# Kernel tuning notes

Hardware: AMD Instinct MI355X
Metric: run time of the kernel (lower is better)

The kernel has to match this reference:

```python
import jax, jax.numpy as jnp
import numpy as np

T, B, I, H = 512, 64, 128, 1024


def setup_inputs() -> dict:
    key = jax.random.key(0)
    k1, k2, k3, k4 = jax.random.split(key, 4)
    # scale recurrent weights to keep tanh in a reasonable regime (spectral-radius-ish)
    return {
        "x": jax.random.normal(k1, (T, B, I), dtype=jnp.float32),
        "h0": jnp.zeros((B, H), dtype=jnp.float32),
        "w_ih": jax.random.normal(k2, (H, I), dtype=jnp.float32) / np.sqrt(I),
        "w_hh": jax.random.normal(k3, (H, H), dtype=jnp.float32) * (0.9 / np.sqrt(H)),
        "b": jax.random.normal(k4, (H,), dtype=jnp.float32) * 0.1,
    }


def reference(x, h0, w_ih, w_hh, b):
    # ESNLayer: python loop over time -> lax.scan with the recurrent carry.
    # cell: h_t = tanh(x_t @ W_ih^T + h_{t-1} @ W_hh^T + b); out_t = h_t
    def step(h, x_t):
        h_new = jnp.tanh(x_t @ w_ih.T + h @ w_hh.T + b)  # [B, H]
        return h_new, h_new

    h_final, outputs = jax.lax.scan(step, h0, x)  # outputs: [T, B, H]
    return outputs, h_final
```

## Files before the change

kernel.cpp:

```cpp
#include <hip/hip_runtime.h>
#include <math.h>


#define T_STEPS 512
#define BATCH   64
#define HDIM    1024
#define IDIM    128
#define KDIM    1152
#define NWG     256
#define NB      8

typedef float f32x4_t __attribute__((ext_vector_type(4)));

__device__ __forceinline__ unsigned sc_load(const unsigned* p) {
    unsigned v;
    asm volatile("global_load_dword %0, %1, off sc0 sc1\n\ts_waitcnt vmcnt(0)"
                 : "=&v"(v) : "v"(p) : "memory");
    return v;
}

__device__ __forceinline__ void sc_load4x4(const float* p0, const float* p1,
                                           const float* p2, const float* p3,
                                           float4& a, float4& b,
                                           float4& c, float4& d) {
    asm volatile(
        "global_load_dwordx4 %0, %4, off sc0 sc1\n\t"
        "global_load_dwordx4 %1, %5, off sc0 sc1\n\t"
        "global_load_dwordx4 %2, %6, off sc0 sc1\n\t"
        "global_load_dwordx4 %3, %7, off sc0 sc1\n\t"
        "s_waitcnt vmcnt(0)"
        : "=&v"(a), "=&v"(b), "=&v"(c), "=&v"(d)
        : "v"(p0), "v"(p1), "v"(p2), "v"(p3)
        : "memory");
}

__device__ __forceinline__ void sc_store4(float* p, float4 v) {
    f32x4_t t;
    t.x = v.x; t.y = v.y; t.z = v.z; t.w = v.w;
    asm volatile("global_store_dwordx4 %0, %1, off sc0 sc1\n\ts_waitcnt vmcnt(0)"
                 :: "v"(p), "v"(t) : "memory");
}

__device__ __forceinline__ void flag_store(unsigned* p, unsigned v) {
    asm volatile("global_store_dword %0, %1, off sc0 sc1"
                 :: "v"(p), "v"(v) : "memory");
}

__global__ void transpose_f32(const float* __restrict__ src, float* __restrict__ dst,
                              int R, int C) {
    __shared__ float tile[64][65];
    const int tcol = threadIdx.x & 63;
    const int trow = threadIdx.x >> 6;
    const int nbx = C >> 6;
    const int bx = blockIdx.x % nbx;
    const int by = blockIdx.x / nbx;
    const int c0 = bx << 6, r0 = by << 6;
    for (int i = trow; i < 64; i += 4)
        tile[i][tcol] = src[(size_t)(r0 + i) * C + c0 + tcol];
    __syncthreads();
    for (int i = trow; i < 64; i += 4)
        dst[(size_t)(c0 + i) * R + r0 + tcol] = tile[tcol][i];
}

__global__ __launch_bounds__(512) void esn_persistent(
    const float* __restrict__ x,
    const float* __restrict__ h0,
    const float* __restrict__ WT,
    const float* __restrict__ bias,
    float* __restrict__ out,
    float* __restrict__ hfin,
    unsigned* flags)
{
    const int tid  = threadIdx.x;
    const int wg   = blockIdx.x;
    const int wave = tid >> 6;
    const int lane = tid & 63;
    const int jq   = lane & 7;
    const int ksub = lane >> 3;
    const int jblk = ((wg & 7) << 2) | ((wg >> 3) & 3);
    const int bgrp = wg >> 5;
    const int b0   = bgrp << 3;
    const int j0   = (jblk << 5) + (jq << 2);
    const int krec = wave << 7;
    const int kx   = HDIM + (wave << 4) + (ksub << 1);

    __shared__ float  ht2[8 * 1024];
    __shared__ float  htx[8 * 128];
    __shared__ float4 red[2][8 * 8 * 9];

    float4 Wv[18];
    {
        const float* wp = WT + (size_t)krec * HDIM + j0;
        #pragma unroll
        for (int i = 0; i < 4; ++i) {
            const int kk = ((i << 3) + ksub) << 2;
            const float* wk = wp + (size_t)kk * HDIM;
            Wv[i * 4 + 0] = *(const float4*)(wk);
            Wv[i * 4 + 1] = *(const float4*)(wk + HDIM);
            Wv[i * 4 + 2] = *(const float4*)(wk + 2 * HDIM);
            Wv[i * 4 + 3] = *(const float4*)(wk + 3 * HDIM);
        }
        const float* wkx = WT + (size_t)kx * HDIM + j0;
        Wv[16] = *(const float4*)(wkx);
        Wv[17] = *(const float4*)(wkx + HDIM);
    }

    float4 b4 = make_float4(0.f, 0.f, 0.f, 0.f);
    int jj = 0;
    if (lane < 8) {
        jj = (jblk << 5) + (lane << 2);
        b4 = *(const float4*)(bias + jj);
    }

    unsigned* fl_pub = flags + (bgrp << 8) + (jblk << 3) + wave;
    const unsigned* fl_poll = flags + (bgrp << 8) + (wave << 5) + (lane & 31);

    const int sbb = lane >> 5;
    const int sko = (lane & 31) << 2;
    float* hdst = ht2 + (wave << 10) + (lane << 2);
    const int xr = lane >> 3;
    const int xco = (lane & 7) << 1;
    float* xdst = htx + (wave << 7) + (xr << 4) + xco;
    const float* hb = ht2 + (wave << 10);
    const float* xb = htx + (wave << 7);

    float2 xv2 = *(const float2*)(x + (size_t)(b0 + xr) * IDIM + (wave << 4) + xco);

    for (int t = 0; t < T_STEPS; ++t) {
        *(float2*)xdst = xv2;
        if (t == 0) {
            const float* p = h0 + (size_t)(b0 + sbb) * HDIM + krec + sko;
            *(float4*)(hdst)       = *(const float4*)(p);
            *(float4*)(hdst + 256) = *(const float4*)(p + 2 * HDIM);
            *(float4*)(hdst + 512) = *(const float4*)(p + 4 * HDIM);
            *(float4*)(hdst + 768) = *(const float4*)(p + 6 * HDIM);
        } else {
            unsigned f;
            do { f = sc_load(fl_poll); } while (!__all((int)(f >= (unsigned)t)));
            const float* p = out + ((size_t)(t - 1) * BATCH + b0 + sbb) * HDIM
                             + krec + sko;
            float4 a, b, c, d;
            sc_load4x4(p, p + 2 * HDIM, p + 4 * HDIM, p + 6 * HDIM, a, b, c, d);
            *(float4*)(hdst)       = a;
            *(float4*)(hdst + 256) = b;
            *(float4*)(hdst + 512) = c;
            *(float4*)(hdst + 768) = d;
        }

        if (t + 1 < T_STEPS)
            xv2 = *(const float2*)(x + ((size_t)(t + 1) * BATCH + b0 + xr) * IDIM
                                   + (wave << 4) + xco);

        float4 acc[NB];
        #pragma unroll
        for (int bb = 0; bb < NB; ++bb) acc[bb] = make_float4(0.f, 0.f, 0.f, 0.f);

        #pragma unroll
        for (int i = 0; i < 4; ++i) {
            const int ko = ((i << 3) + ksub) << 2;
            const float4 w0 = Wv[i * 4 + 0], w1 = Wv[i * 4 + 1];
            const float4 w2 = Wv[i * 4 + 2], w3 = Wv[i * 4 + 3];
            #pragma unroll
            for (int bb = 0; bb < NB; ++bb) {
                float4 h4 = *(const float4*)(hb + (bb << 7) + ko);
                acc[bb].x = fmaf(w0.x, h4.x, acc[bb].x);
                acc[bb].y = fmaf(w0.y, h4.x, acc[bb].y);
                acc[bb].z = fmaf(w0.z, h4.x, acc[bb].z);
                acc[bb].w = fmaf(w0.w, h4.x, acc[bb].w);
                acc[bb].x = fmaf(w1.x, h4.y, acc[bb].x);
                acc[bb].y = fmaf(w1.y, h4.y, acc[bb].y);
                acc[bb].z = fmaf(w1.z, h4.y, acc[bb].z);
                acc[bb].w = fmaf(w1.w, h4.y, acc[bb].w);
                acc[bb].x = fmaf(w2.x, h4.z, acc[bb].x);
                acc[bb].y = fmaf(w2.y, h4.z, acc[bb].y);
                acc[bb].z = fmaf(w2.z, h4.z, acc[bb].z);
                acc[bb].w = fmaf(w2.w, h4.z, acc[bb].w);
                acc[bb].x = fmaf(w3.x, h4.w, acc[bb].x);
                acc[bb].y = fmaf(w3.y, h4.w, acc[bb].y);
                acc[bb].z = fmaf(w3.z, h4.w, acc[bb].z);
                acc[bb].w = fmaf(w3.w, h4.w, acc[bb].w);
            }
        }
        #pragma unroll
        for (int bb = 0; bb < NB; ++bb) {
            float2 hx = *(const float2*)(xb + (bb << 4) + (ksub << 1));
            acc[bb].x = fmaf(Wv[16].x, hx.x, acc[bb].x);
            acc[bb].y = fmaf(Wv[16].y, hx.x, acc[bb].y);
            acc[bb].z = fmaf(Wv[16].z, hx.x, acc[bb].z);
            acc[bb].w = fmaf(Wv[16].w, hx.x, acc[bb].w);
            acc[bb].x = fmaf(Wv[17].x, hx.y, acc[bb].x);
            acc[bb].y = fmaf(Wv[17].y, hx.y, acc[bb].y);
            acc[bb].z = fmaf(Wv[17].z, hx.y, acc[bb].z);
            acc[bb].w = fmaf(Wv[17].w, hx.y, acc[bb].w);
        }

        #pragma unroll
        for (int bb = 0; bb < NB; ++bb) {
            acc[bb].x += __shfl_xor(acc[bb].x, 8);
            acc[bb].y += __shfl_xor(acc[bb].y, 8);
            acc[bb].z += __shfl_xor(acc[bb].z, 8);
            acc[bb].w += __shfl_xor(acc[bb].w, 8);
            acc[bb].x += __shfl_xor(acc[bb].x, 16);
            acc[bb].y += __shfl_xor(acc[bb].y, 16);
            acc[bb].z += __shfl_xor(acc[bb].z, 16);
            acc[bb].w += __shfl_xor(acc[bb].w, 16);
            acc[bb].x += __shfl_xor(acc[bb].x, 32);
            acc[bb].y += __shfl_xor(acc[bb].y, 32);
            acc[bb].z += __shfl_xor(acc[bb].z, 32);
            acc[bb].w += __shfl_xor(acc[bb].w, 32);
        }
        if (ksub == 0) {
            #pragma unroll
            for (int bb = 0; bb < NB; ++bb)
                red[t & 1][((wave << 3) + jq) * 9 + bb] = acc[bb];
        }
        __syncthreads();

        if (lane < 8) {
            float4 s = make_float4(0.f, 0.f, 0.f, 0.f);
            #pragma unroll
            for (int w = 0; w < 8; ++w) {
                float4 r = red[t & 1][((w << 3) + lane) * 9 + wave];
                s.x += r.x; s.y += r.y; s.z += r.z; s.w += r.w;
            }
            float4 o;
            o.x = tanhf(s.x + b4.x);
            o.y = tanhf(s.y + b4.y);
            o.z = tanhf(s.z + b4.z);
            o.w = tanhf(s.w + b4.w);
            sc_store4(out + ((size_t)t * BATCH + b0 + wave) * HDIM + jj, o);
            if (t == T_STEPS - 1)
                *(float4*)(hfin + (size_t)(b0 + wave) * HDIM + jj) = o;
        }
        if (lane == 0)
            flag_store(fl_pub, (unsigned)(t + 1));
    }
}

extern "C" void kernel_launch(void* const* d_in, const int* in_sizes, int n_in,
                              void* d_out, int out_size, void* d_ws, size_t ws_size,
                              hipStream_t stream) {
    const float* x    = (const float*)d_in[0];
    const float* h0   = (const float*)d_in[1];
    const float* w_ih = (const float*)d_in[2];
    const float* w_hh = (const float*)d_in[3];
    const float* bias = (const float*)d_in[4];
    float* out = (float*)d_out;

    char* ws = (char*)d_ws;
    float*    WT    = (float*)ws;
    unsigned* flags = (unsigned*)(ws + 4718592);

    (void)hipMemsetAsync(flags, 0, 8192, stream);
    transpose_f32<<<256, 256, 0, stream>>>(w_hh, WT, HDIM, HDIM);
    transpose_f32<<<32, 256, 0, stream>>>(w_ih, WT + (size_t)HDIM * HDIM, HDIM, IDIM);
    esn_persistent<<<NWG, 512, 0, stream>>>(x, h0, WT, bias,
                                            out, out + (size_t)T_STEPS * BATCH * HDIM,
                                            flags);
}
```

Before: 3.115 ms.

## Use L2-scoped coherence when a batch group's workgroups share one XCD

Workgroups are remapped so each batch group is wg&7, which under round-robin dispatch likely places all 32 workgroups of a group on the same XCD. At startup each group records its XCC IDs through atomics. If they all share one XCD, the flag polls, hidden-state loads and output stores use sc0-only (L2-coherent) accesses instead of sc0 sc1 system-scope bypass, which cuts per-step synchronisation latency. Flag stores are issued twice, and every 16th poll still uses full bypass as a safety net. This adds a startup barrier, extra workspace, and relies on the assumption about hardware dispatch order.

After: 8.399 ms. 2.7x slower.

```diff
diff --git a/kernel.cpp b/kernel.cpp
--- a/kernel.cpp
+++ b/kernel.cpp
@@ -12,38 +12,62 @@
 
 typedef float f32x4_t __attribute__((ext_vector_type(4)));
 
-__device__ __forceinline__ unsigned sc_load(const unsigned* p) {
+__device__ __forceinline__ unsigned flag_load(const unsigned* p, bool slow) {
     unsigned v;
-    asm volatile("global_load_dword %0, %1, off sc0 sc1\n\ts_waitcnt vmcnt(0)"
-                 : "=&v"(v) : "v"(p) : "memory");
+    if (slow)
+        asm volatile("global_load_dword %0, %1, off sc0 sc1\n\ts_waitcnt vmcnt(0)"
+                     : "=&v"(v) : "v"(p) : "memory");
+    else
+        asm volatile("global_load_dword %0, %1, off sc0\n\ts_waitcnt vmcnt(0)"
+                     : "=&v"(v) : "v"(p) : "memory");
     return v;
 }
 
-__device__ __forceinline__ void sc_load4x4(const float* p0, const float* p1,
-                                           const float* p2, const float* p3,
-                                           float4& a, float4& b,
-                                           float4& c, float4& d) {
-    asm volatile(
-        "global_load_dwordx4 %0, %4, off sc0 sc1\n\t"
-        "global_load_dwordx4 %1, %5, off sc0 sc1\n\t"
-        "global_load_dwordx4 %2, %6, off sc0 sc1\n\t"
-        "global_load_dwordx4 %3, %7, off sc0 sc1\n\t"
-        "s_waitcnt vmcnt(0)"
-        : "=&v"(a), "=&v"(b), "=&v"(c), "=&v"(d)
-        : "v"(p0), "v"(p1), "v"(p2), "v"(p3)
-        : "memory");
-}
-
-__device__ __forceinline__ void sc_store4(float* p, float4 v) {
+__device__ __forceinline__ void h_load4x4(const float* p0, const float* p1,
+                                          const float* p2, const float* p3,
+                                          float4& a, float4& b,
+                                          float4& c, float4& d, bool byp) {
+    if (byp)
+        asm volatile(
+            "global_load_dwordx4 %0, %4, off sc0 sc1\n\t"
+            "global_load_dwordx4 %1, %5, off sc0 sc1\n\t"
+            "global_load_dwordx4 %2, %6, off sc0 sc1\n\t"
+            "global_load_dwordx4 %3, %7, off sc0 sc1\n\t"
+            "s_waitcnt vmcnt(0)"
+            : "=&v"(a), "=&v"(b), "=&v"(c), "=&v"(d)
+            : "v"(p0), "v"(p1), "v"(p2), "v"(p3)
+            : "memory");
+    else
+        asm volatile(
+            "global_load_dwordx4 %0, %4, off sc0\n\t"
+            "global_load_dwordx4 %1, %5, off sc0\n\t"
+            "global_load_dwordx4 %2, %6, off sc0\n\t"
+            "global_load_dwordx4 %3, %7, off sc0\n\t"
+            "s_waitcnt vmcnt(0)"
+            : "=&v"(a), "=&v"(b), "=&v"(c), "=&v"(d)
+            : "v"(p0), "v"(p1), "v"(p2), "v"(p3)
+            : "memory");
+}
+
+__device__ __forceinline__ void out_store4(float* p, float4 v, bool byp) {
     f32x4_t t;
     t.x = v.x; t.y = v.y; t.z = v.z; t.w = v.w;
-    asm volatile("global_store_dwordx4 %0, %1, off sc0 sc1\n\ts_waitcnt vmcnt(0)"
-                 :: "v"(p), "v"(t) : "memory");
-}
-
-__device__ __forceinline__ void flag_store(unsigned* p, unsigned v) {
-    asm volatile("global_store_dword %0, %1, off sc0 sc1"
-                 :: "v"(p), "v"(v) : "memory");
+    if (byp)
+        asm volatile("global_store_dwordx4 %0, %1, off sc0 sc1\n\ts_waitcnt vmcnt(0)"
+                     :: "v"(p), "v"(t) : "memory");
+    else
+        asm volatile("global_store_dwordx4 %0, %1, off sc0\n\ts_waitcnt vmcnt(0)"
+                     :: "v"(p), "v"(t) : "memory");
+}
+
+__device__ __forceinline__ void flag_store(unsigned* p, unsigned v, bool byp) {
+    if (byp)
+        asm volatile("global_store_dword %0, %1, off sc0 sc1"
+                     :: "v"(p), "v"(v) : "memory");
+    else
+        asm volatile("global_store_dword %0, %1, off sc0\n\t"
+                     "global_store_dword %0, %1, off sc0 sc1"
+                     :: "v"(p), "v"(v) : "memory");
 }
 
 __global__ void transpose_f32(const float* __restrict__ src, float* __restrict__ dst,
@@ -77,8 +101,8 @@
     const int lane = tid & 63;
     const int jq   = lane & 7;
     const int ksub = lane >> 3;
-    const int jblk = ((wg & 7) << 2) | ((wg >> 3) & 3);
-    const int bgrp = wg >> 5;
+    const int bgrp = wg & 7;
+    const int jblk = wg >> 3;
     const int b0   = bgrp << 3;
     const int j0   = (jblk << 5) + (jq << 2);
     const int krec = wave << 7;
@@ -87,6 +111,25 @@
     __shared__ float  ht2[8 * 1024];
     __shared__ float  htx[8 * 128];
     __shared__ float4 red[2][8 * 8 * 9];
+    __shared__ int    fast_sh;
+
+    unsigned* vmask = flags + 2048;
+    unsigned* vcnt  = flags + 2056;
+    if (tid == 0) {
+        unsigned xcd;
+        asm volatile("s_getreg_b32 %0, hwreg(HW_REG_XCC_ID)" : "=s"(xcd));
+        __hip_atomic_fetch_or(&vmask[bgrp], 1u << (xcd & 7), __ATOMIC_RELAXED,
+                              __HIP_MEMORY_SCOPE_AGENT);
+        __hip_atomic_fetch_add(&vcnt[bgrp], 1u, __ATOMIC_RELEASE,
+                               __HIP_MEMORY_SCOPE_AGENT);
+        while (__hip_atomic_load(&vcnt[bgrp], __ATOMIC_ACQUIRE,
+                                 __HIP_MEMORY_SCOPE_AGENT) < 32u) {}
+        unsigned m = __hip_atomic_load(&vmask[bgrp], __ATOMIC_RELAXED,
+                                       __HIP_MEMORY_SCOPE_AGENT);
+        fast_sh = (__popc(m) == 1);
+    }
+    __syncthreads();
+    const bool byp = (fast_sh == 0);
 
     float4 Wv[18];
     {
@@ -135,12 +178,16 @@
             *(float4*)(hdst + 512) = *(const float4*)(p + 4 * HDIM);
             *(float4*)(hdst + 768) = *(const float4*)(p + 6 * HDIM);
         } else {
-            unsigned f;
-            do { f = sc_load(fl_poll); } while (!__all((int)(f >= (unsigned)t)));
+            unsigned n = 0, f;
+            do {
+                ++n;
+                f = flag_load(fl_poll, byp || ((n & 15u) == 0u));
+            } while (!__all((int)(f >= (unsigned)t)));
             const float* p = out + ((size_t)(t - 1) * BATCH + b0 + sbb) * HDIM
                              + krec + sko;
             float4 a, b, c, d;
-            sc_load4x4(p, p + 2 * HDIM, p + 4 * HDIM, p + 6 * HDIM, a, b, c, d);
+            h_load4x4(p, p + 2 * HDIM, p + 4 * HDIM, p + 6 * HDIM,
+                      a, b, c, d, byp);
             *(float4*)(hdst)       = a;
             *(float4*)(hdst + 256) = b;
             *(float4*)(hdst + 512) = c;
@@ -228,12 +275,12 @@
             o.y = tanhf(s.y + b4.y);
             o.z = tanhf(s.z + b4.z);
             o.w = tanhf(s.w + b4.w);
-            sc_store4(out + ((size_t)t * BATCH + b0 + wave) * HDIM + jj, o);
+            out_store4(out + ((size_t)t * BATCH + b0 + wave) * HDIM + jj, o, byp);
             if (t == T_STEPS - 1)
                 *(float4*)(hfin + (size_t)(b0 + wave) * HDIM + jj) = o;
         }
         if (lane == 0)
-            flag_store(fl_pub, (unsigned)(t + 1));
+            flag_store(fl_pub, (unsigned)(t + 1), byp);
     }
 }
 
@@ -251,7 +298,7 @@
     float*    WT    = (float*)ws;
     unsigned* flags = (unsigned*)(ws + 4718592);
 
-    (void)hipMemsetAsync(flags, 0, 8192, stream);
+    (void)hipMemsetAsync(flags, 0, 8192 + 128, stream);
     transpose_f32<<<256, 256, 0, stream>>>(w_hh, WT, HDIM, HDIM);
     transpose_f32<<<32, 256, 0, stream>>>(w_ih, WT + (size_t)HDIM * HDIM, HDIM, IDIM);
     esn_persistent<<<NWG, 512, 0, stream>>>(x, h0, WT, bias,
```

## Replace flag-based step sync with poison-sentinel polling on output data

Applied to the files above, without the earlier changes.

Drops the per-wave flag publish/poll handshake. Consumers now spin directly on the previous step's hidden-state rows in the output buffer until no element equals a poison pattern, and the output buffer is memset to that pattern beforehand. This removes a flag round-trip and the store drain on the producer side, so data and synchronization travel together. It adds a 128 MB memset per call. Correctness relies on tanh never producing the poison bit pattern and on each 16-byte store becoming visible as a unit.

Result: faster. 2.767 ms (-11.2%).

```diff
diff --git a/kernel.cpp b/kernel.cpp
--- a/kernel.cpp
+++ b/kernel.cpp
@@ -9,15 +9,9 @@
 #define KDIM    1152
 #define NWG     256
 #define NB      8
+#define POISON  0x7F7F7F7Fu
 
 typedef float f32x4_t __attribute__((ext_vector_type(4)));
-
-__device__ __forceinline__ unsigned sc_load(const unsigned* p) {
-    unsigned v;
-    asm volatile("global_load_dword %0, %1, off sc0 sc1\n\ts_waitcnt vmcnt(0)"
-                 : "=&v"(v) : "v"(p) : "memory");
-    return v;
-}
 
 __device__ __forceinline__ void sc_load4x4(const float* p0, const float* p1,
                                            const float* p2, const float* p3,
@@ -34,16 +28,18 @@
         : "memory");
 }
 
-__device__ __forceinline__ void sc_store4(float* p, float4 v) {
+__device__ __forceinline__ void sc_store4_nodrain(float* p, float4 v) {
     f32x4_t t;
     t.x = v.x; t.y = v.y; t.z = v.z; t.w = v.w;
-    asm volatile("global_store_dwordx4 %0, %1, off sc0 sc1\n\ts_waitcnt vmcnt(0)"
+    asm volatile("global_store_dwordx4 %0, %1, off sc0 sc1"
                  :: "v"(p), "v"(t) : "memory");
 }
 
-__device__ __forceinline__ void flag_store(unsigned* p, unsigned v) {
-    asm volatile("global_store_dword %0, %1, off sc0 sc1"
-                 :: "v"(p), "v"(v) : "memory");
+__device__ __forceinline__ unsigned chk4(float4 v) {
+    return (unsigned)((__float_as_uint(v.x) == POISON) |
+                      (__float_as_uint(v.y) == POISON) |
+                      (__float_as_uint(v.z) == POISON) |
+                      (__float_as_uint(v.w) == POISON));
 }
 
 __global__ void transpose_f32(const float* __restrict__ src, float* __restrict__ dst,
@@ -68,8 +64,7 @@
     const float* __restrict__ WT,
     const float* __restrict__ bias,
     float* __restrict__ out,
-    float* __restrict__ hfin,
-    unsigned* flags)
+    float* __restrict__ hfin)
 {
     const int tid  = threadIdx.x;
     const int wg   = blockIdx.x;
@@ -112,9 +107,6 @@
         b4 = *(const float4*)(bias + jj);
     }
 
-    unsigned* fl_pub = flags + (bgrp << 8) + (jblk << 3) + wave;
-    const unsigned* fl_poll = flags + (bgrp << 8) + (wave << 5) + (lane & 31);
-
     const int sbb = lane >> 5;
     const int sko = (lane & 31) << 2;
     float* hdst = ht2 + (wave << 10) + (lane << 2);
@@ -135,12 +127,13 @@
             *(float4*)(hdst + 512) = *(const float4*)(p + 4 * HDIM);
             *(float4*)(hdst + 768) = *(const float4*)(p + 6 * HDIM);
         } else {
-            unsigned f;
-            do { f = sc_load(fl_poll); } while (!__all((int)(f >= (unsigned)t)));
             const float* p = out + ((size_t)(t - 1) * BATCH + b0 + sbb) * HDIM
                              + krec + sko;
             float4 a, b, c, d;
-            sc_load4x4(p, p + 2 * HDIM, p + 4 * HDIM, p + 6 * HDIM, a, b, c, d);
+            do {
+                sc_load4x4(p, p + 2 * HDIM, p + 4 * HDIM, p + 6 * HDIM,
+                           a, b, c, d);
+            } while (__any((int)(chk4(a) | chk4(b) | chk4(c) | chk4(d))));
             *(float4*)(hdst)       = a;
             *(float4*)(hdst + 256) = b;
             *(float4*)(hdst + 512) = c;
@@ -228,12 +221,10 @@
             o.y = tanhf(s.y + b4.y);
             o.z = tanhf(s.z + b4.z);
             o.w = tanhf(s.w + b4.w);
-            sc_store4(out + ((size_t)t * BATCH + b0 + wave) * HDIM + jj, o);
+            sc_store4_nodrain(out + ((size_t)t * BATCH + b0 + wave) * HDIM + jj, o);
             if (t == T_STEPS - 1)
                 *(float4*)(hfin + (size_t)(b0 + wave) * HDIM + jj) = o;
         }
-        if (lane == 0)
-            flag_store(fl_pub, (unsigned)(t + 1));
     }
 }
 
@@ -248,13 +239,12 @@
     float* out = (float*)d_out;
 
     char* ws = (char*)d_ws;
-    float*    WT    = (float*)ws;
-    unsigned* flags = (unsigned*)(ws + 4718592);
-
-    (void)hipMemsetAsync(flags, 0, 8192, stream);
+    float* WT = (float*)ws;
+
+    (void)hipMemsetAsync(out, 0x7F,
+                         (size_t)T_STEPS * BATCH * HDIM * sizeof(float), stream);
     transpose_f32<<<256, 256, 0, stream>>>(w_hh, WT, HDIM, HDIM);
     transpose_f32<<<32, 256, 0, stream>>>(w_ih, WT + (size_t)HDIM * HDIM, HDIM, IDIM);
     esn_persistent<<<NWG, 512, 0, stream>>>(x, h0, WT, bias,
-                                            out, out + (size_t)T_STEPS * BATCH * HDIM,
-                                            flags);
-}
+                                            out, out + (size_t)T_STEPS * BATCH * HDIM);
+}
```
